# Optimization experiments

Hardware: AMD Instinct MI355X
Metric: run time of the kernel (lower is better)

The kernel has to match this reference:

```python
import jax, jax.numpy as jnp
import numpy as np

LN_EPS = 1e-5


def layer_norm(x, g, b):
    mu = jnp.mean(x, axis=-1, keepdims=True)
    var = jnp.var(x, axis=-1, keepdims=True)
    return (x - mu) / jnp.sqrt(var + LN_EPS) * g + b


def balanced_assignment(scores):
    # scores: [T, E]. Assign exactly C = T//E tokens to each expert,
    # greedily per expert by affinity (emulates libbase.balanced_assignment's
    # equal-split output structure deterministically).
    T, E = scores.shape
    C = T // E
    taken = jnp.zeros((T,), dtype=bool)
    parts = []
    for e in range(E):  # small fixed loop over experts
        s = jnp.where(taken, -jnp.inf, scores[:, e])
        _, idx = jax.lax.top_k(s, C)
        parts.append(idx)
        taken = taken.at[idx].set(True)
    return jnp.concatenate(parts)  # [T], chunks of C tokens per expert


def setup_inputs() -> dict:
    key = jax.random.key(0)
    ks = jax.random.split(key, 4)
    B, S, D, F, E = 4, 2048, 1024, 4096, 8
    return {
        "x": jax.random.normal(ks[0], (B, S, D), dtype=jnp.float32),
        "centroids": jax.random.normal(ks[1], (E, D), dtype=jnp.float32) * 0.1,
        "ln_g": jnp.ones((D,), dtype=jnp.float32),
        "ln_b": jnp.zeros((D,), dtype=jnp.float32),
        "w1": jax.random.normal(ks[2], (E, D, F), dtype=jnp.float32) * 0.02,
        "b1": jnp.zeros((E, F), dtype=jnp.float32),
        "w2": jax.random.normal(ks[3], (E, F, D), dtype=jnp.float32) * 0.02,
        "b2": jnp.zeros((E, D), dtype=jnp.float32),
    }


def reference(x, centroids, ln_g, ln_b, w1, b1, w2, b2):
    D = x.shape[-1]
    feat = x.reshape(-1, D)                      # [T, D]
    T = feat.shape[0]
    E = centroids.shape[0]
    C = T // E

    # affinity scores under no_grad in the original
    norm = layer_norm(feat, ln_g, ln_b)
    scores = jax.lax.stop_gradient(norm @ centroids.T)   # [T, E]

    sort_by_expert = balanced_assignment(scores)          # [T]

    routed = feat[sort_by_expert].reshape(E, C, D)        # dispatch gather

    # expert FFN sublayer: residual + W2(gelu(W1(ln(x))))
    h = layer_norm(routed, ln_g, ln_b)
    h = jax.nn.gelu(jnp.einsum('ecd,edf->ecf', h, w1) + b1[:, None, :])
    h = jnp.einsum('ecf,efd->ecd', h, w2) + b2[:, None, :]
    out = routed + h                                      # [E, C, D]

    # inverse_sort scatter: undo the dispatch permutation
    inv = jnp.zeros((T,), dtype=jnp.int32).at[sort_by_expert].set(
        jnp.arange(T, dtype=jnp.int32))
    return out.reshape(T, D)[inv].reshape(x.shape)
```

## Files before the change

### kernel.cpp

```cpp
#include <hip/hip_runtime.h>
#include <hip/hip_bf16.h>
#include <stdint.h>


#define T_TOK 8192
#define DM    1024
#define FF    4096
#define NE    8
#define CAP   1024

typedef __attribute__((ext_vector_type(8))) __bf16 bf16x8;
typedef __attribute__((ext_vector_type(4))) float  f32x4;

__device__ __forceinline__ unsigned short f2bf(float f) {
  unsigned u = __float_as_uint(f);
  u += 0x7FFFu + ((u >> 16) & 1u);
  return (unsigned short)(u >> 16);
}
__device__ __forceinline__ void gload_lds16(const void* g, void* l) {
  __builtin_amdgcn_global_load_lds(
      (const __attribute__((address_space(1))) unsigned int*)(uintptr_t)g,
      (__attribute__((address_space(3))) unsigned int*)l, 16, 0, 0);
}

__global__ __launch_bounds__(256) void ln_scores_k(
    const float* __restrict__ x, const float* __restrict__ g,
    const float* __restrict__ b, const float* __restrict__ cent,
    unsigned short* __restrict__ nrm, float* __restrict__ scores) {
  const int t = blockIdx.x, tid = threadIdx.x;
  const int lane = tid & 63, w = tid >> 6;
  float4 v = ((const float4*)(x + (size_t)t * DM))[tid];
  float f0 = v.x, f1 = v.y, f2 = v.z, f3 = v.w;
  float s = f0 + f1 + f2 + f3;
  float sq = f0 * f0 + f1 * f1 + f2 * f2 + f3 * f3;
#pragma unroll
  for (int o = 32; o > 0; o >>= 1) { s += __shfl_xor(s, o); sq += __shfl_xor(sq, o); }
  __shared__ float red[8];
  if (lane == 0) { red[w] = s; red[4 + w] = sq; }
  __syncthreads();
  float S = red[0] + red[1] + red[2] + red[3];
  float SQ = red[4] + red[5] + red[6] + red[7];
  float mu = S * (1.0f / DM);
  float var = SQ * (1.0f / DM) - mu * mu;
  float rstd = rsqrtf(var + 1e-5f);
  float4 gv = ((const float4*)g)[tid];
  float4 bv = ((const float4*)b)[tid];
  float n0 = (f0 - mu) * rstd * gv.x + bv.x;
  float n1 = (f1 - mu) * rstd * gv.y + bv.y;
  float n2 = (f2 - mu) * rstd * gv.z + bv.z;
  float n3 = (f3 - mu) * rstd * gv.w + bv.w;
  ushort4 o4;
  o4.x = f2bf(n0); o4.y = f2bf(n1); o4.z = f2bf(n2); o4.w = f2bf(n3);
  ((ushort4*)(nrm + (size_t)t * DM))[tid] = o4;
  __shared__ float sred[4];
  for (int e = 0; e < NE; ++e) {
    float4 cv = ((const float4*)(cent + e * DM))[tid];
    float p = n0 * cv.x + n1 * cv.y + n2 * cv.z + n3 * cv.w;
#pragma unroll
    for (int o = 32; o > 0; o >>= 1) p += __shfl_xor(p, o);
    if (lane == 0) sred[w] = p;
    __syncthreads();
    if (tid == 0) scores[(size_t)e * T_TOK + t] = sred[0] + sred[1] + sred[2] + sred[3];
    __syncthreads();
  }
}

__device__ __forceinline__ void pivot_scan(const unsigned* hist, unsigned* S) {
  const int l = threadIdx.x;
  unsigned v0 = hist[4 * l], v1 = hist[4 * l + 1];
  unsigned v2 = hist[4 * l + 2], v3 = hist[4 * l + 3];
  unsigned own = v0 + v1 + v2 + v3;
  unsigned s = own;
#pragma unroll
  for (int off = 1; off < 64; off <<= 1) {
    unsigned t = __shfl_down(s, off);
    if (l + off < 64) s += t;
  }
  unsigned i3 = (s - own) + v3;
  unsigned i2 = i3 + v2;
  unsigned i1 = i2 + v1;
  unsigned i0 = i1 + v0;
  unsigned need = S[0];
  if (i0 >= need && i0 - v0 < need) { S[1] = 4 * l + 0; S[0] = need - (i0 - v0); }
  if (i1 >= need && i1 - v1 < need) { S[1] = 4 * l + 1; S[0] = need - (i1 - v1); }
  if (i2 >= need && i2 - v2 < need) { S[1] = 4 * l + 2; S[0] = need - (i2 - v2); }
  if (i3 >= need && i3 - v3 < need) { S[1] = 4 * l + 3; S[0] = need - (i3 - v3); }
}
__device__ __forceinline__ void tie_select(const unsigned* bmap, unsigned* S,
                                           int* tokdst, unsigned char* taken) {
  const int l = threadIdx.x;
  unsigned wds[4] = {bmap[4 * l], bmap[4 * l + 1], bmap[4 * l + 2], bmap[4 * l + 3]};
  unsigned cnt = __popc(wds[0]) + __popc(wds[1]) + __popc(wds[2]) + __popc(wds[3]);
  unsigned p = cnt;
#pragma unroll
  for (int off = 1; off < 64; off <<= 1) {
    unsigned t = __shfl_up(p, off);
    if (l >= off) p += t;
  }
  unsigned base = p - cnt;
  const unsigned r = S[0];
#pragma unroll
  for (int c = 0; c < 4; ++c) {
    unsigned word = wds[c];
    while (word && base < r) {
      int b = __ffs(word) - 1; word &= word - 1;
      int i = (4 * l + c) * 32 + b;
      unsigned pp = atomicAdd(&S[2], 1u);
      tokdst[pp] = i; taken[i] = 1;
      ++base;
    }
    base += __popc(word);
  }
}

__device__ void assign_body(const float* __restrict__ scores,
                            int* __restrict__ tok, char* smem) {
  unsigned*       key   = (unsigned*)smem;
  unsigned short* candA = (unsigned short*)(smem + 32768);
  unsigned short* candB = (unsigned short*)(smem + 49152);
  unsigned char*  taken = (unsigned char*)(smem + 65536);
  unsigned*       hist  = (unsigned*)(smem + 73728);
  unsigned*       bmap  = (unsigned*)(smem + 74752);
  unsigned*       S     = (unsigned*)(smem + 75776);
  const int tid = threadIdx.x;
  for (int i = tid; i < T_TOK; i += 1024) taken[i] = 0;
  __syncthreads();
  for (int e = 0; e < NE; ++e) {
    const float* se = scores + (size_t)e * T_TOK;
    if (tid < 256) hist[tid] = 0;
    if (tid == 0) { S[0] = CAP; S[2] = 0; S[4] = 0; }
    __syncthreads();
#pragma unroll
    for (int j = 0; j < 8; ++j) {
      int i = j * 1024 + tid;
      unsigned k = 0;
      if (!taken[i]) {
        unsigned bb = __float_as_uint(se[i]);
        k = (bb & 0x80000000u) ? ~bb : (bb | 0x80000000u);
      }
      key[i] = k;
      atomicAdd(&hist[k >> 24], 1u);
    }
    __syncthreads();
    if (tid < 64) pivot_scan(hist, S);
    __syncthreads();
    {
      const unsigned pb = S[1];
#pragma unroll
      for (int j = 0; j < 8; ++j) {
        int i = j * 1024 + tid;
        unsigned by = key[i] >> 24;
        if (by > pb) {
          unsigned p = atomicAdd(&S[2], 1u);
          tok[e * CAP + p] = i; taken[i] = 1;
        } else if (by == pb) {
          unsigned q = atomicAdd(&S[4], 1u);
          candA[q] = (unsigned short)i;
        }
      }
    }
    __syncthreads();
    unsigned short* cur = candA;
    unsigned short* nxt = candB;
    for (int shift = 16; shift >= 0; shift -= 8) {
      const unsigned m = S[4];
      __syncthreads();
      if (tid < 256) hist[tid] = 0;
      if (tid == 0) S[4] = 0;
      __syncthreads();
      for (unsigned q = tid; q < m; q += 1024)
        atomicAdd(&hist[(key[cur[q]] >> shift) & 255u], 1u);
      __syncthreads();
      if (tid < 64) pivot_scan(hist, S);
      __syncthreads();
      const unsigned pb = S[1];
      for (unsigned q = tid; q < m; q += 1024) {
        unsigned i = cur[q];
        unsigned by = (key[i] >> shift) & 255u;
        if (by > pb) {
          unsigned p = atomicAdd(&S[2], 1u);
          tok[e * CAP + p] = (int)i; taken[i] = 1;
        } else if (by == pb) {
          unsigned t2 = atomicAdd(&S[4], 1u);
          nxt[t2] = (unsigned short)i;
        }
      }
      __syncthreads();
      unsigned short* tmp = cur; cur = nxt; nxt = tmp;
    }
    if (tid < 256) bmap[tid] = 0;
    __syncthreads();
    {
      const unsigned m = S[4];
      for (unsigned q = tid; q < m; q += 1024) {
        unsigned i = cur[q];
        atomicOr(&bmap[i >> 5], 1u << (i & 31));
      }
    }
    __syncthreads();
    if (tid < 64) tie_select(bmap, S, tok + e * CAP, taken);
    __syncthreads();
  }
}

__global__ __launch_bounds__(1024) void fat_assign_transpose(
    const float* __restrict__ scores, int* __restrict__ tok,
    const float* __restrict__ w1, const float* __restrict__ w2,
    unsigned short* __restrict__ w1T, unsigned short* __restrict__ w2T) {
  __shared__ __align__(16) char smem[77824];
  if (blockIdx.x == 0) { assign_body(scores, tok, smem); return; }
  const int tix = blockIdx.x - 1;
  const int which = tix >> 11;
  const int r = tix & 2047;
  const int e = r >> 8;
  const int rr = r & 255;
  int K, N, nt, kt;
  const float* s;
  unsigned short* d;
  if (which == 0) { K = DM; N = FF; nt = rr & 31; kt = rr >> 5; s = w1; d = w1T; }
  else            { K = FF; N = DM; nt = rr & 7;  kt = rr >> 3; s = w2; d = w2T; }
  s += (size_t)e * K * N;
  d += (size_t)e * N * K;
  const int q = threadIdx.x >> 8, t2 = threadIdx.x & 255;
  const int k0 = kt * 128 + (q >> 1) * 64;
  const int n0 = nt * 128 + (q & 1) * 64;
  float (*t)[65] = (float (*)[65])(smem + q * 16640);
  for (int p = t2; p < 1024; p += 256) {
    int rw = p >> 4, c4 = (p & 15) * 4;
    float4 v = *(const float4*)(s + (size_t)(k0 + rw) * N + n0 + c4);
    t[c4 + 0][rw] = v.x; t[c4 + 1][rw] = v.y;
    t[c4 + 2][rw] = v.z; t[c4 + 3][rw] = v.w;
  }
  __syncthreads();
  for (int p = t2; p < 512; p += 256) {
    int c = p >> 3, r8 = (p & 7) * 8;
    unsigned short tmp[8];
#pragma unroll
    for (int i = 0; i < 8; ++i) tmp[i] = f2bf(t[c][r8 + i]);
    *(uint4*)(d + (size_t)(n0 + c) * K + k0 + r8) = *(const uint4*)tmp;
  }
}

template <int EPI, bool GATHER, int K, int N, int BN, int WM, int WN>
__global__ __launch_bounds__(512, 2) void gemm_8ph(
    const unsigned short* __restrict__ A, const unsigned short* __restrict__ Bt,
    const float* __restrict__ bias, const int* __restrict__ tok,
    const float* __restrict__ xres, void* __restrict__ Cout) {
  constexpr int BM = 256;
  constexpr int NT = K / 64;
  constexpr int NITER = NT / 2;
  constexpr int RM = BM / WM, RN = BN / WN;
  constexpr int MR = RM / 16, NR = RN / 16, MH = MR / 2;
  constexpr int ALD = 2;
  constexpr int BLD = BN / 128;
  constexpr int ASH = BM * 32;
  constexpr int BSH = BN * 32;
  constexpr int BUFS = 2 * ASH + 2 * BSH;
  __shared__ __align__(16) unsigned short lds[2 * BUFS];
  __shared__ int tokl[BM];

  const int flat = blockIdx.x + gridDim.x * (blockIdx.y + gridDim.y * blockIdx.z);
  const int nwg = gridDim.x * gridDim.y * gridDim.z;
  const int nf = (flat & 7) * (nwg >> 3) + (flat >> 3);
  const int bx = nf % gridDim.x;
  const int rem = nf / gridDim.x;
  const int e  = rem / gridDim.y;
  const int n0 = bx * BN, m0 = (rem % gridDim.y) * BM;

  const int tid = threadIdx.x, lane = tid & 63, w = tid >> 6;
  const int wr = w / WN, wc = w % WN;
  const int lr = lane & 15, lk = lane >> 4;

  for (int i = tid; i < BM; i += 512) tokl[i] = tok[e * CAP + m0 + i];
  __syncthreads();

  const unsigned short* aptr[ALD];
  const unsigned short* bptr[BLD];
  const unsigned short* Be = Bt + (size_t)e * N * K + (size_t)n0 * K;
#pragma unroll
  for (int i = 0; i < ALD; ++i) {
    int c = i * 512 + tid, row = c >> 2, sp = c & 3;
    int s = sp ^ ((row >> 1) & 3);
    size_t grow = GATHER ? (size_t)tokl[row] : (size_t)(e * CAP + m0 + row);
    aptr[i] = A + grow * K + s * 8;
  }
#pragma unroll
  for (int i = 0; i < BLD; ++i) {
    int c = i * 512 + tid, row = c >> 2, sp = c & 3;
    int s = sp ^ ((row >> 1) & 3);
    bptr[i] = Be + (size_t)row * K + s * 8;
  }
  auto stageA = [&](int tile, int kh) {
#pragma unroll
    for (int i = 0; i < ALD; ++i)
      gload_lds16(aptr[i] + tile * 64 + kh * 32,
                  lds + (size_t)(tile & 1) * BUFS + kh * ASH + (i * 512 + tid) * 8);
  };
  auto stageB = [&](int tile, int kh) {
#pragma unroll
    for (int i = 0; i < BLD; ++i)
      gload_lds16(bptr[i] + tile * 64 + kh * 32,
                  lds + (size_t)(tile & 1) * BUFS + 2 * ASH + kh * BSH + (i * 512 + tid) * 8);
  };

  const int swz = (lr >> 1) & 3;
  const int afo = (wr * RM + lr) * 32 + (lk ^ swz) * 8;
  const int bfo = (wc * RN + lr) * 32 + (lk ^ swz) * 8;

  f32x4 acc[MR][NR] = {};

  stageA(0, 0); stageB(0, 0); stageA(0, 1); stageB(0, 1);
  stageA(1, 0); stageB(1, 0);
  asm volatile("s_waitcnt vmcnt(%0)" :: "i"(ALD + BLD) : "memory");
  __builtin_amdgcn_s_barrier();

#pragma unroll 1
  for (int it = 0; it < NITER; ++it) {
    const int ta = 2 * it, tb = 2 * it + 1;
    bf16x8 bfr[NR], af[MH];
#pragma unroll
    for (int p = 0; p < 8; ++p) {
      const int buf = p >> 2, kh = (p >> 1) & 1, mh = p & 1;
      if (mh == 0) {
#pragma unroll
        for (int ni = 0; ni < NR; ++ni)
          bfr[ni] = *(const bf16x8*)(lds + (size_t)buf * BUFS + 2 * ASH +
                                     kh * BSH + bfo + ni * 512);
      }
#pragma unroll
      for (int j = 0; j < MH; ++j)
        af[j] = *(const bf16x8*)(lds + (size_t)buf * BUFS + kh * ASH + afo +
                                 (mh * MH + j) * 512);
      if (p == 0)      {                       stageA(tb, 1);     stageB(tb, 1); }
      else if (p == 2) { if (ta + 2 < NT)      stageA(ta + 2, 0); }
      else if (p == 3) { if (ta + 2 < NT)      stageB(ta + 2, 0); }
      else if (p == 4) { if (ta + 2 < NT)    { stageA(ta + 2, 1); stageB(ta + 2, 1); } }
      else if (p == 6) { if (tb + 2 < NT)      stageA(tb + 2, 0); }
      else if (p == 7) { if (tb + 2 < NT)      stageB(tb + 2, 0); }
      if (p == 3 || p == 7)
        asm volatile("s_waitcnt vmcnt(%0)" :: "i"(ALD + BLD) : "memory");
      __builtin_amdgcn_s_barrier();
      asm volatile("s_waitcnt lgkmcnt(0)" ::: "memory");
      __builtin_amdgcn_sched_barrier(0);
      __builtin_amdgcn_s_setprio(1);
#pragma unroll
      for (int j = 0; j < MH; ++j)
#pragma unroll
        for (int ni = 0; ni < NR; ++ni)
          acc[mh * MH + j][ni] = __builtin_amdgcn_mfma_f32_16x16x32_bf16(
              af[j], bfr[ni], acc[mh * MH + j][ni], 0, 0, 0);
      __builtin_amdgcn_s_setprio(0);
      __builtin_amdgcn_s_barrier();
    }
  }

  const int lg = lane >> 4;
#pragma unroll
  for (int ni = 0; ni < NR; ++ni) {
    const int n = n0 + wc * RN + ni * 16 + lr;
    const float bb = bias[e * N + n];
#pragma unroll
    for (int mi = 0; mi < MR; ++mi) {
#pragma unroll
      for (int r = 0; r < 4; ++r) {
        const int ml = wr * RM + mi * 16 + lg * 4 + r;
        float v = acc[mi][ni][r] + bb;
        if (EPI == 1) {
          float z = 1.5957691216f * v + 0.07135481283f * v * v * v;
          float gl = v / (1.0f + __expf(-z));
          ((unsigned short*)Cout)[(size_t)(e * CAP + m0 + ml) * N + n] = f2bf(gl);
        } else {
          const int token = tokl[ml];
          v += xres[(size_t)token * DM + n];
          ((float*)Cout)[(size_t)token * (size_t)N + n] = v;
        }
      }
    }
  }
}

extern "C" void kernel_launch(void* const* d_in, const int* in_sizes, int n_in,
                              void* d_out, int out_size, void* d_ws, size_t ws_size,
                              hipStream_t stream) {
  const float* x    = (const float*)d_in[0];
  const float* cent = (const float*)d_in[1];
  const float* ln_g = (const float*)d_in[2];
  const float* ln_b = (const float*)d_in[3];
  const float* w1   = (const float*)d_in[4];
  const float* b1   = (const float*)d_in[5];
  const float* w2   = (const float*)d_in[6];
  const float* b2   = (const float*)d_in[7];
  float* out = (float*)d_out;

  char* ws = (char*)d_ws;
  size_t off = 0;
  unsigned short* w1T = (unsigned short*)(ws + off); off += (size_t)NE * FF * DM * 2;
  unsigned short* w2T = (unsigned short*)(ws + off); off += (size_t)NE * DM * FF * 2;
  unsigned short* nrm = (unsigned short*)(ws + off); off += (size_t)T_TOK * DM * 2;
  unsigned short* h1  = (unsigned short*)(ws + off); off += (size_t)T_TOK * FF * 2;
  float* scores       = (float*)(ws + off);          off += (size_t)NE * T_TOK * 4;
  int* tok            = (int*)(ws + off);            off += (size_t)T_TOK * 4;

  ln_scores_k<<<dim3(T_TOK), 256, 0, stream>>>(x, ln_g, ln_b, cent, nrm, scores);
  fat_assign_transpose<<<dim3(1 + 4096), 1024, 0, stream>>>(
      scores, tok, w1, w2, w1T, w2T);
  gemm_8ph<1, true, DM, FF, 256, 2, 4>
      <<<dim3(FF / 256, CAP / 256, NE), 512, 0, stream>>>(nrm, w1T, b1, tok, nullptr, h1);
  gemm_8ph<2, false, FF, DM, 128, 4, 2>
      <<<dim3(DM / 128, CAP / 256, NE), 512, 0, stream>>>(h1, w2T, b2, tok, x, out);
}
```

Measured before the change: 346.7 us.

## Restructure GEMM main loop from 8 half-phases to 4 full phases

The bf16 MFMA GEMM loop now runs four phases per two-tile iteration instead of eight. Each phase loads all A and B fragments for one k-half, issues one combined A+B stage, and waits with a deeper vmcnt so two stages stay in flight. The last iteration is peeled with explicit drain waits. This halves the barrier and wait overhead per tile but raises register pressure, since all MR A fragments are live at once, and it shortens the prefetch distance.

```diff
diff --git a/kernel.cpp b/kernel.cpp
--- a/kernel.cpp
+++ b/kernel.cpp
@@ -21,6 +21,9 @@
   __builtin_amdgcn_global_load_lds(
       (const __attribute__((address_space(1))) unsigned int*)(uintptr_t)g,
       (__attribute__((address_space(3))) unsigned int*)l, 16, 0, 0);
+}
+template <int NN> __device__ __forceinline__ void vmw() {
+  asm volatile("s_waitcnt vmcnt(%0)" :: "i"(NN) : "memory");
 }
 
 __global__ __launch_bounds__(256) void ln_scores_k(
@@ -242,7 +245,7 @@
 }
 
 template <int EPI, bool GATHER, int K, int N, int BN, int WM, int WN>
-__global__ __launch_bounds__(512, 2) void gemm_8ph(
+__global__ __launch_bounds__(512, 2) void gemm_4ph(
     const unsigned short* __restrict__ A, const unsigned short* __restrict__ Bt,
     const float* __restrict__ bias, const int* __restrict__ tok,
     const float* __restrict__ xres, void* __restrict__ Cout) {
@@ -250,9 +253,11 @@
   constexpr int NT = K / 64;
   constexpr int NITER = NT / 2;
   constexpr int RM = BM / WM, RN = BN / WN;
-  constexpr int MR = RM / 16, NR = RN / 16, MH = MR / 2;
+  constexpr int MR = RM / 16, NR = RN / 16;
   constexpr int ALD = 2;
   constexpr int BLD = BN / 128;
+  constexpr int LD  = ALD + BLD;
+  constexpr int VMN = 2 * LD;
   constexpr int ASH = BM * 32;
   constexpr int BSH = BN * 32;
   constexpr int BUFS = 2 * ASH + 2 * BSH;
@@ -290,13 +295,11 @@
     int s = sp ^ ((row >> 1) & 3);
     bptr[i] = Be + (size_t)row * K + s * 8;
   }
-  auto stageA = [&](int tile, int kh) {
+  auto stage = [&](int tile, int kh) {
 #pragma unroll
     for (int i = 0; i < ALD; ++i)
       gload_lds16(aptr[i] + tile * 64 + kh * 32,
                   lds + (size_t)(tile & 1) * BUFS + kh * ASH + (i * 512 + tid) * 8);
-  };
-  auto stageB = [&](int tile, int kh) {
 #pragma unroll
     for (int i = 0; i < BLD; ++i)
       gload_lds16(bptr[i] + tile * 64 + kh * 32,
@@ -309,48 +312,53 @@
 
   f32x4 acc[MR][NR] = {};
 
-  stageA(0, 0); stageB(0, 0); stageA(0, 1); stageB(0, 1);
-  stageA(1, 0); stageB(1, 0);
-  asm volatile("s_waitcnt vmcnt(%0)" :: "i"(ALD + BLD) : "memory");
+  auto phase = [&](int buf, int kh, bool dostage, int st, int sk, int vmv) {
+    bf16x8 af[MR], bfr[NR];
+#pragma unroll
+    for (int ni = 0; ni < NR; ++ni)
+      bfr[ni] = *(const bf16x8*)(lds + (size_t)buf * BUFS + 2 * ASH +
+                                 kh * BSH + bfo + ni * 512);
+#pragma unroll
+    for (int mi = 0; mi < MR; ++mi)
+      af[mi] = *(const bf16x8*)(lds + (size_t)buf * BUFS + kh * ASH + afo +
+                                mi * 512);
+    if (dostage) stage(st, sk);
+    if (vmv == 0) vmw<0>();
+    else if (vmv == 3) vmw<3>();
+    else if (vmv == 4) vmw<4>();
+    else if (vmv == 6) vmw<6>();
+    else vmw<8>();
+    __builtin_amdgcn_s_barrier();
+    asm volatile("s_waitcnt lgkmcnt(0)" ::: "memory");
+    __builtin_amdgcn_sched_barrier(0);
+    __builtin_amdgcn_s_setprio(1);
+#pragma unroll
+    for (int mi = 0; mi < MR; ++mi)
+#pragma unroll
+      for (int ni = 0; ni < NR; ++ni)
+        acc[mi][ni] = __builtin_amdgcn_mfma_f32_16x16x32_bf16(
+            af[mi], bfr[ni], acc[mi][ni], 0, 0, 0);
+    __builtin_amdgcn_s_setprio(0);
+    __builtin_amdgcn_s_barrier();
+  };
+
+  stage(0, 0); stage(0, 1); stage(1, 0);
+  vmw<VMN>();
   __builtin_amdgcn_s_barrier();
 
 #pragma unroll 1
   for (int it = 0; it < NITER; ++it) {
-    const int ta = 2 * it, tb = 2 * it + 1;
-    bf16x8 bfr[NR], af[MH];
-#pragma unroll
-    for (int p = 0; p < 8; ++p) {
-      const int buf = p >> 2, kh = (p >> 1) & 1, mh = p & 1;
-      if (mh == 0) {
-#pragma unroll
-        for (int ni = 0; ni < NR; ++ni)
-          bfr[ni] = *(const bf16x8*)(lds + (size_t)buf * BUFS + 2 * ASH +
-                                     kh * BSH + bfo + ni * 512);
-      }
-#pragma unroll
-      for (int j = 0; j < MH; ++j)
-        af[j] = *(const bf16x8*)(lds + (size_t)buf * BUFS + kh * ASH + afo +
-                                 (mh * MH + j) * 512);
-      if (p == 0)      {                       stageA(tb, 1);     stageB(tb, 1); }
-      else if (p == 2) { if (ta + 2 < NT)      stageA(ta + 2, 0); }
-      else if (p == 3) { if (ta + 2 < NT)      stageB(ta + 2, 0); }
-      else if (p == 4) { if (ta + 2 < NT)    { stageA(ta + 2, 1); stageB(ta + 2, 1); } }
-      else if (p == 6) { if (tb + 2 < NT)      stageA(tb + 2, 0); }
-      else if (p == 7) { if (tb + 2 < NT)      stageB(tb + 2, 0); }
-      if (p == 3 || p == 7)
-        asm volatile("s_waitcnt vmcnt(%0)" :: "i"(ALD + BLD) : "memory");
-      __builtin_amdgcn_s_barrier();
-      asm volatile("s_waitcnt lgkmcnt(0)" ::: "memory");
-      __builtin_amdgcn_sched_barrier(0);
-      __builtin_amdgcn_s_setprio(1);
-#pragma unroll
-      for (int j = 0; j < MH; ++j)
-#pragma unroll
-        for (int ni = 0; ni < NR; ++ni)
-          acc[mh * MH + j][ni] = __builtin_amdgcn_mfma_f32_16x16x32_bf16(
-              af[j], bfr[ni], acc[mh * MH + j][ni], 0, 0, 0);
-      __builtin_amdgcn_s_setprio(0);
-      __builtin_amdgcn_s_barrier();
+    const int ta = 2 * it, tb = ta + 1;
+    if (it + 1 < NITER) {
+      phase(0, 0, true, tb, 1, VMN);
+      phase(0, 1, true, ta + 2, 0, VMN);
+      phase(1, 0, true, ta + 2, 1, VMN);
+      phase(1, 1, true, tb + 2, 0, VMN);
+    } else {
+      phase(0, 0, true, tb, 1, VMN);
+      phase(0, 1, false, 0, 0, LD);
+      phase(1, 0, false, 0, 0, 0);
+      phase(1, 1, false, 0, 0, 0);
     }
   }
 
@@ -404,8 +412,8 @@
   ln_scores_k<<<dim3(T_TOK), 256, 0, stream>>>(x, ln_g, ln_b, cent, nrm, scores);
   fat_assign_transpose<<<dim3(1 + 4096), 1024, 0, stream>>>(
       scores, tok, w1, w2, w1T, w2T);
-  gemm_8ph<1, true, DM, FF, 256, 2, 4>
+  gemm_4ph<1, true, DM, FF, 256, 2, 4>
       <<<dim3(FF / 256, CAP / 256, NE), 512, 0, stream>>>(nrm, w1T, b1, tok, nullptr, h1);
-  gemm_8ph<2, false, FF, DM, 128, 4, 2>
+  gemm_4ph<2, false, FF, DM, 128, 4, 2>
       <<<dim3(DM / 128, CAP / 256, NE), 512, 0, stream>>>(h1, w2T, b2, tok, x, out);
 }
```

Result: slower. 551.4 us (+59.0%).

## Split second expert GEMM along K and add combine kernel

Applied to the files above, without the earlier changes.

The down-projection GEMM is split into two K halves, doubling the workgroup count, and writes fp32 partials to workspace. A new combine kernel sums the partials, adds bias and residual, and scatters rows to token positions. This targets low occupancy of the single-wave grid at the cost of extra partial-sum memory traffic and an added launch. It falls back to the fused path if the workspace is too small.

```diff
diff --git a/kernel.cpp b/kernel.cpp
--- a/kernel.cpp
+++ b/kernel.cpp
@@ -241,7 +241,7 @@
   }
 }
 
-template <int EPI, bool GATHER, int K, int N, int BN, int WM, int WN>
+template <int EPI, bool GATHER, int K, int LDA, int N, int BN, int WM, int WN>
 __global__ __launch_bounds__(512, 2) void gemm_8ph(
     const unsigned short* __restrict__ A, const unsigned short* __restrict__ Bt,
     const float* __restrict__ bias, const int* __restrict__ tok,
@@ -264,31 +264,36 @@
   const int nf = (flat & 7) * (nwg >> 3) + (flat >> 3);
   const int bx = nf % gridDim.x;
   const int rem = nf / gridDim.x;
-  const int e  = rem / gridDim.y;
+  const int zz = rem / gridDim.y;
+  const int e  = (EPI == 3) ? (zz >> 1) : zz;
+  const int ks = (EPI == 3) ? (zz & 1) : 0;
+  const int koff = ks * K;
   const int n0 = bx * BN, m0 = (rem % gridDim.y) * BM;
 
   const int tid = threadIdx.x, lane = tid & 63, w = tid >> 6;
   const int wr = w / WN, wc = w % WN;
   const int lr = lane & 15, lk = lane >> 4;
 
-  for (int i = tid; i < BM; i += 512) tokl[i] = tok[e * CAP + m0 + i];
-  __syncthreads();
+  if (GATHER || EPI == 2) {
+    for (int i = tid; i < BM; i += 512) tokl[i] = tok[e * CAP + m0 + i];
+    __syncthreads();
+  }
 
   const unsigned short* aptr[ALD];
   const unsigned short* bptr[BLD];
-  const unsigned short* Be = Bt + (size_t)e * N * K + (size_t)n0 * K;
+  const unsigned short* Be = Bt + (size_t)e * N * LDA + (size_t)n0 * LDA + koff;
 #pragma unroll
   for (int i = 0; i < ALD; ++i) {
     int c = i * 512 + tid, row = c >> 2, sp = c & 3;
     int s = sp ^ ((row >> 1) & 3);
     size_t grow = GATHER ? (size_t)tokl[row] : (size_t)(e * CAP + m0 + row);
-    aptr[i] = A + grow * K + s * 8;
+    aptr[i] = A + grow * LDA + koff + s * 8;
   }
 #pragma unroll
   for (int i = 0; i < BLD; ++i) {
     int c = i * 512 + tid, row = c >> 2, sp = c & 3;
     int s = sp ^ ((row >> 1) & 3);
-    bptr[i] = Be + (size_t)row * K + s * 8;
+    bptr[i] = Be + (size_t)row * LDA + s * 8;
   }
   auto stageA = [&](int tile, int kh) {
 #pragma unroll
@@ -317,6 +322,7 @@
 #pragma unroll 1
   for (int it = 0; it < NITER; ++it) {
     const int ta = 2 * it, tb = 2 * it + 1;
+    const bool last = (it + 1 == NITER);
     bf16x8 bfr[NR], af[MH];
 #pragma unroll
     for (int p = 0; p < 8; ++p) {
@@ -337,8 +343,12 @@
       else if (p == 4) { if (ta + 2 < NT)    { stageA(ta + 2, 1); stageB(ta + 2, 1); } }
       else if (p == 6) { if (tb + 2 < NT)      stageA(tb + 2, 0); }
       else if (p == 7) { if (tb + 2 < NT)      stageB(tb + 2, 0); }
-      if (p == 3 || p == 7)
-        asm volatile("s_waitcnt vmcnt(%0)" :: "i"(ALD + BLD) : "memory");
+      if (p == 3) {
+        if (last) asm volatile("s_waitcnt vmcnt(0)" ::: "memory");
+        else      asm volatile("s_waitcnt vmcnt(%0)" :: "i"(ALD + BLD) : "memory");
+      } else if (p == 7) {
+        if (!last) asm volatile("s_waitcnt vmcnt(%0)" :: "i"(ALD + BLD) : "memory");
+      }
       __builtin_amdgcn_s_barrier();
       asm volatile("s_waitcnt lgkmcnt(0)" ::: "memory");
       __builtin_amdgcn_sched_barrier(0);
@@ -358,7 +368,7 @@
 #pragma unroll
   for (int ni = 0; ni < NR; ++ni) {
     const int n = n0 + wc * RN + ni * 16 + lr;
-    const float bb = bias[e * N + n];
+    const float bb = (EPI == 3) ? 0.0f : bias[e * N + n];
 #pragma unroll
     for (int mi = 0; mi < MR; ++mi) {
 #pragma unroll
@@ -369,14 +379,37 @@
           float z = 1.5957691216f * v + 0.07135481283f * v * v * v;
           float gl = v / (1.0f + __expf(-z));
           ((unsigned short*)Cout)[(size_t)(e * CAP + m0 + ml) * N + n] = f2bf(gl);
-        } else {
+        } else if (EPI == 2) {
           const int token = tokl[ml];
           v += xres[(size_t)token * DM + n];
           ((float*)Cout)[(size_t)token * (size_t)N + n] = v;
+        } else {
+          const size_t row = (size_t)ks * T_TOK + e * CAP + m0 + ml;
+          ((float*)Cout)[row * (size_t)N + n] = v;
         }
       }
     }
   }
+}
+
+__global__ __launch_bounds__(256) void combine_k(
+    const float* __restrict__ part, const int* __restrict__ tok,
+    const float* __restrict__ b2, const float* __restrict__ x,
+    float* __restrict__ out) {
+  const int r = blockIdx.x;
+  const int e = r >> 10;
+  const int token = tok[r];
+  const int d4 = threadIdx.x;
+  float4 p0 = ((const float4*)(part + (size_t)r * DM))[d4];
+  float4 p1 = ((const float4*)(part + (size_t)(T_TOK + r) * DM))[d4];
+  float4 bb = ((const float4*)(b2 + (size_t)e * DM))[d4];
+  float4 xx = ((const float4*)(x + (size_t)token * DM))[d4];
+  float4 o;
+  o.x = p0.x + p1.x + bb.x + xx.x;
+  o.y = p0.y + p1.y + bb.y + xx.y;
+  o.z = p0.z + p1.z + bb.z + xx.z;
+  o.w = p0.w + p1.w + bb.w + xx.w;
+  ((float4*)(out + (size_t)token * DM))[d4] = o;
 }
 
 extern "C" void kernel_launch(void* const* d_in, const int* in_sizes, int n_in,
@@ -400,12 +433,21 @@
   unsigned short* h1  = (unsigned short*)(ws + off); off += (size_t)T_TOK * FF * 2;
   float* scores       = (float*)(ws + off);          off += (size_t)NE * T_TOK * 4;
   int* tok            = (int*)(ws + off);            off += (size_t)T_TOK * 4;
+  float* part         = (float*)(ws + off);          off += (size_t)2 * T_TOK * DM * 4;
+  const bool use_split = (ws_size >= off);
 
   ln_scores_k<<<dim3(T_TOK), 256, 0, stream>>>(x, ln_g, ln_b, cent, nrm, scores);
   fat_assign_transpose<<<dim3(1 + 4096), 1024, 0, stream>>>(
       scores, tok, w1, w2, w1T, w2T);
-  gemm_8ph<1, true, DM, FF, 256, 2, 4>
+  gemm_8ph<1, true, DM, DM, FF, 256, 2, 4>
       <<<dim3(FF / 256, CAP / 256, NE), 512, 0, stream>>>(nrm, w1T, b1, tok, nullptr, h1);
-  gemm_8ph<2, false, FF, DM, 128, 4, 2>
-      <<<dim3(DM / 128, CAP / 256, NE), 512, 0, stream>>>(h1, w2T, b2, tok, x, out);
-}
+  if (use_split) {
+    gemm_8ph<3, false, FF / 2, FF, DM, 128, 4, 2>
+        <<<dim3(DM / 128, CAP / 256, NE * 2), 512, 0, stream>>>(
+            h1, w2T, nullptr, tok, nullptr, part);
+    combine_k<<<dim3(T_TOK), 256, 0, stream>>>(part, tok, b2, x, out);
+  } else {
+    gemm_8ph<2, false, FF, FF, DM, 128, 4, 2>
+        <<<dim3(DM / 128, CAP / 256, NE), 512, 0, stream>>>(h1, w2T, b2, tok, x, out);
+  }
+}
```

After: 356.8 us. 2.9% more time.

## Move W2 transpose into first GEMM's tail blocks to overlap with compute

Applied to the files above, without the earlier changes.

The W2 fp32-to-bf16 transpose is taken out of the assignment/transpose kernel and appended as extra workgroups on the first expert GEMM launch. It now runs alongside GEMM1 rather than before it, which shortens the serial transpose kernel. The GEMM is changed to a flat 1D grid with compile-time grid dims, and the final loop iteration drains vmcnt fully at phase 3 instead of waiting at phase 7. The tail blocks reuse the GEMM's LDS and run with 512 threads, and they compete with GEMM tiles for CU slots.

```diff
diff --git a/kernel.cpp b/kernel.cpp
--- a/kernel.cpp
+++ b/kernel.cpp
@@ -203,31 +203,24 @@
   }
 }
 
-__global__ __launch_bounds__(1024) void fat_assign_transpose(
+__global__ __launch_bounds__(1024) void fat_assign_w1t(
     const float* __restrict__ scores, int* __restrict__ tok,
-    const float* __restrict__ w1, const float* __restrict__ w2,
-    unsigned short* __restrict__ w1T, unsigned short* __restrict__ w2T) {
+    const float* __restrict__ w1, unsigned short* __restrict__ w1T) {
   __shared__ __align__(16) char smem[77824];
   if (blockIdx.x == 0) { assign_body(scores, tok, smem); return; }
   const int tix = blockIdx.x - 1;
-  const int which = tix >> 11;
-  const int r = tix & 2047;
-  const int e = r >> 8;
-  const int rr = r & 255;
-  int K, N, nt, kt;
-  const float* s;
-  unsigned short* d;
-  if (which == 0) { K = DM; N = FF; nt = rr & 31; kt = rr >> 5; s = w1; d = w1T; }
-  else            { K = FF; N = DM; nt = rr & 7;  kt = rr >> 3; s = w2; d = w2T; }
-  s += (size_t)e * K * N;
-  d += (size_t)e * N * K;
+  const int e = tix >> 8;
+  const int rr = tix & 255;
+  const int nt = rr & 31, kt = rr >> 5;
+  const float* s = w1 + (size_t)e * DM * FF;
+  unsigned short* d = w1T + (size_t)e * FF * DM;
   const int q = threadIdx.x >> 8, t2 = threadIdx.x & 255;
   const int k0 = kt * 128 + (q >> 1) * 64;
   const int n0 = nt * 128 + (q & 1) * 64;
   float (*t)[65] = (float (*)[65])(smem + q * 16640);
   for (int p = t2; p < 1024; p += 256) {
     int rw = p >> 4, c4 = (p & 15) * 4;
-    float4 v = *(const float4*)(s + (size_t)(k0 + rw) * N + n0 + c4);
+    float4 v = *(const float4*)(s + (size_t)(k0 + rw) * FF + n0 + c4);
     t[c4 + 0][rw] = v.x; t[c4 + 1][rw] = v.y;
     t[c4 + 2][rw] = v.z; t[c4 + 3][rw] = v.w;
   }
@@ -237,15 +230,17 @@
     unsigned short tmp[8];
 #pragma unroll
     for (int i = 0; i < 8; ++i) tmp[i] = f2bf(t[c][r8 + i]);
-    *(uint4*)(d + (size_t)(n0 + c) * K + k0 + r8) = *(const uint4*)tmp;
-  }
-}
-
-template <int EPI, bool GATHER, int K, int N, int BN, int WM, int WN>
+    *(uint4*)(d + (size_t)(n0 + c) * DM + k0 + r8) = *(const uint4*)tmp;
+  }
+}
+
+template <int EPI, bool GATHER, int K, int N, int BN, int WM, int WN,
+          int GX, int GY, int GZ, bool TWTAIL>
 __global__ __launch_bounds__(512, 2) void gemm_8ph(
     const unsigned short* __restrict__ A, const unsigned short* __restrict__ Bt,
     const float* __restrict__ bias, const int* __restrict__ tok,
-    const float* __restrict__ xres, void* __restrict__ Cout) {
+    const float* __restrict__ xres, void* __restrict__ Cout,
+    const float* __restrict__ tsrc, unsigned short* __restrict__ tdst) {
   constexpr int BM = 256;
   constexpr int NT = K / 64;
   constexpr int NITER = NT / 2;
@@ -256,16 +251,44 @@
   constexpr int ASH = BM * 32;
   constexpr int BSH = BN * 32;
   constexpr int BUFS = 2 * ASH + 2 * BSH;
+  constexpr int NW = GX * GY * GZ;
   __shared__ __align__(16) unsigned short lds[2 * BUFS];
   __shared__ int tokl[BM];
 
-  const int flat = blockIdx.x + gridDim.x * (blockIdx.y + gridDim.y * blockIdx.z);
-  const int nwg = gridDim.x * gridDim.y * gridDim.z;
-  const int nf = (flat & 7) * (nwg >> 3) + (flat >> 3);
-  const int bx = nf % gridDim.x;
-  const int rem = nf / gridDim.x;
-  const int e  = rem / gridDim.y;
-  const int n0 = bx * BN, m0 = (rem % gridDim.y) * BM;
+  if (TWTAIL && (int)blockIdx.x >= NW) {
+    const int tix = blockIdx.x - NW;
+    const int e = tix >> 8;
+    const int rr = tix & 255;
+    const int nt = rr & 7, kt = rr >> 3;
+    const float* s = tsrc + (size_t)e * FF * DM;
+    unsigned short* d = tdst + (size_t)e * DM * FF;
+    const int q = threadIdx.x >> 7, t2 = threadIdx.x & 127;
+    const int k0 = kt * 128 + (q >> 1) * 64;
+    const int n0 = nt * 128 + (q & 1) * 64;
+    float (*t)[65] = (float (*)[65])((char*)lds + q * 16640);
+    for (int p = t2; p < 1024; p += 128) {
+      int rw = p >> 4, c4 = (p & 15) * 4;
+      float4 v = *(const float4*)(s + (size_t)(k0 + rw) * DM + n0 + c4);
+      t[c4 + 0][rw] = v.x; t[c4 + 1][rw] = v.y;
+      t[c4 + 2][rw] = v.z; t[c4 + 3][rw] = v.w;
+    }
+    __syncthreads();
+    for (int p = t2; p < 512; p += 128) {
+      int c = p >> 3, r8 = (p & 7) * 8;
+      unsigned short tmp[8];
+#pragma unroll
+      for (int i = 0; i < 8; ++i) tmp[i] = f2bf(t[c][r8 + i]);
+      *(uint4*)(d + (size_t)(n0 + c) * FF + k0 + r8) = *(const uint4*)tmp;
+    }
+    return;
+  }
+
+  const int flat = blockIdx.x;
+  const int nf = (flat & 7) * (NW >> 3) + (flat >> 3);
+  const int bx = nf % GX;
+  const int rem = nf / GX;
+  const int e  = rem / GY;
+  const int n0 = bx * BN, m0 = (rem % GY) * BM;
 
   const int tid = threadIdx.x, lane = tid & 63, w = tid >> 6;
   const int wr = w / WN, wc = w % WN;
@@ -317,6 +340,7 @@
 #pragma unroll 1
   for (int it = 0; it < NITER; ++it) {
     const int ta = 2 * it, tb = 2 * it + 1;
+    const bool last = (it + 1 == NITER);
     bf16x8 bfr[NR], af[MH];
 #pragma unroll
     for (int p = 0; p < 8; ++p) {
@@ -337,8 +361,12 @@
       else if (p == 4) { if (ta + 2 < NT)    { stageA(ta + 2, 1); stageB(ta + 2, 1); } }
       else if (p == 6) { if (tb + 2 < NT)      stageA(tb + 2, 0); }
       else if (p == 7) { if (tb + 2 < NT)      stageB(tb + 2, 0); }
-      if (p == 3 || p == 7)
-        asm volatile("s_waitcnt vmcnt(%0)" :: "i"(ALD + BLD) : "memory");
+      if (p == 3) {
+        if (last) asm volatile("s_waitcnt vmcnt(0)" ::: "memory");
+        else      asm volatile("s_waitcnt vmcnt(%0)" :: "i"(ALD + BLD) : "memory");
+      } else if (p == 7) {
+        if (!last) asm volatile("s_waitcnt vmcnt(%0)" :: "i"(ALD + BLD) : "memory");
+      }
       __builtin_amdgcn_s_barrier();
       asm volatile("s_waitcnt lgkmcnt(0)" ::: "memory");
       __builtin_amdgcn_sched_barrier(0);
@@ -402,10 +430,9 @@
   int* tok            = (int*)(ws + off);            off += (size_t)T_TOK * 4;
 
   ln_scores_k<<<dim3(T_TOK), 256, 0, stream>>>(x, ln_g, ln_b, cent, nrm, scores);
-  fat_assign_transpose<<<dim3(1 + 4096), 1024, 0, stream>>>(
-      scores, tok, w1, w2, w1T, w2T);
-  gemm_8ph<1, true, DM, FF, 256, 2, 4>
-      <<<dim3(FF / 256, CAP / 256, NE), 512, 0, stream>>>(nrm, w1T, b1, tok, nullptr, h1);
-  gemm_8ph<2, false, FF, DM, 128, 4, 2>
-      <<<dim3(DM / 128, CAP / 256, NE), 512, 0, stream>>>(h1, w2T, b2, tok, x, out);
-}
+  fat_assign_w1t<<<dim3(1 + 2048), 1024, 0, stream>>>(scores, tok, w1, w1T);
+  gemm_8ph<1, true, DM, FF, 256, 2, 4, FF / 256, CAP / 256, NE, true>
+      <<<dim3(512 + 2048), 512, 0, stream>>>(nrm, w1T, b1, tok, nullptr, h1, w2, w2T);
+  gemm_8ph<2, false, FF, DM, 128, 4, 2, DM / 128, CAP / 256, NE, false>
+      <<<dim3(256), 512, 0, stream>>>(h1, w2T, b2, tok, x, out, nullptr, nullptr);
+}
```

Measured after the change: 382.8 us. 10.4% more time.
